# Kernel tuning notes

Hardware: AMD Instinct MI355X
Metric: run time of the kernel (lower is better)

## Reference

```python
import jax, jax.numpy as jnp
import numpy as np

NEG_SLOPE = 0.2


def setup_inputs() -> dict:
    key = jax.random.key(0)
    ks = jax.random.split(key, 12)
    N, D = 50000, 256
    H, C = 4, 128          # heads, per-head channels; H*C = gnn_hidden_dim = 512
    E = 800000
    edge_index = jax.random.randint(ks[0], (2, E), 0, N, dtype=jnp.int64)
    edge_weight = jax.random.uniform(ks[1], (E,), dtype=jnp.float32)
    s = 1.0 / np.sqrt(D)
    return {
        'edge_index': edge_index,
        'edge_weight': edge_weight,
        'emb':     jax.random.normal(ks[2], (N, D), jnp.float32),
        'W':       jax.random.normal(ks[3], (D, H * C), jnp.float32) * s,
        'att_src': jax.random.normal(ks[4], (H, C), jnp.float32) * s,
        'att_dst': jax.random.normal(ks[5], (H, C), jnp.float32) * s,
        'att_edge': jax.random.normal(ks[6], (H, C), jnp.float32) * s,
        'W_edge':  jax.random.normal(ks[7], (1, H * C), jnp.float32),
        'bias':    jnp.zeros((H * C,), jnp.float32),
        'W_out':   jax.random.normal(ks[8], (H * C, D), jnp.float32) * s,
        'b_out':   jnp.zeros((D,), jnp.float32),
    }


def reference(edge_index, edge_weight, emb, W, att_src, att_dst, att_edge,
              W_edge, bias, W_out, b_out):
    N, D = emb.shape
    H, C = att_src.shape
    src, dst = edge_index[0], edge_index[1]
    E = src.shape[0]

    # GATConv: shared linear projection for src and dst (in_channels is int)
    x = (emb @ W).reshape(N, H, C)                     # [N,H,C]

    # add self loops; edge_attr for loops = per-dst mean of incoming edge_attr
    ones = jnp.ones((E,), emb.dtype)
    cnt = jax.ops.segment_sum(ones, dst, num_segments=N)
    ea_mean = jax.ops.segment_sum(edge_weight, dst, num_segments=N) / jnp.maximum(cnt, 1.0)
    loop = jnp.arange(N, dtype=src.dtype)
    src_f = jnp.concatenate([src, loop])
    dst_f = jnp.concatenate([dst, loop])
    ea = jnp.concatenate([edge_weight, ea_mean])[:, None]   # [E+N, 1]

    e_feat = (ea @ W_edge).reshape(-1, H, C)            # [E+N,H,C]

    a_src = jnp.einsum('nhc,hc->nh', x, att_src)        # [N,H]
    a_dst = jnp.einsum('nhc,hc->nh', x, att_dst)
    a_e = jnp.einsum('ehc,hc->eh', e_feat, att_edge)    # [E+N,H]

    alpha = jax.nn.leaky_relu(a_src[src_f] + a_dst[dst_f] + a_e, NEG_SLOPE)
    # segment softmax over destination neighborhoods
    m = jax.ops.segment_max(alpha, dst_f, num_segments=N)
    alpha = jnp.exp(alpha - m[dst_f])
    denom = jax.ops.segment_sum(alpha, dst_f, num_segments=N)
    alpha = alpha / (denom[dst_f] + 1e-16)              # [E+N,H]

    msg = x[src_f] * alpha[..., None]                   # [E+N,H,C]
    out = jax.ops.segment_sum(msg, dst_f, num_segments=N).reshape(N, H * C) + bias

    return out @ W_out + b_out                          # [N,D]
```

## Files before the change

### kernel.cpp

```cpp
#include <hip/hip_runtime.h>
#include <cstdint>
#include <cstddef>

#define NEG_SLOPE 0.2f
#define HC 512
#define NH 4
#define CAP 64

typedef __attribute__((ext_vector_type(8))) short bf16x8;
typedef __attribute__((ext_vector_type(4))) float f32x4;

__device__ inline float lrelu(float z) { return z > 0.f ? z : NEG_SLOPE * z; }

__device__ inline unsigned short f2bf(float f) {
    unsigned u = __float_as_uint(f);
    u += 0x7FFFu + ((u >> 16) & 1u);
    return (unsigned short)(u >> 16);
}
__device__ inline float bflo(unsigned v) { return __uint_as_float(v << 16); }
__device__ inline float bfhi(unsigned v) { return __uint_as_float(v & 0xffff0000u); }

#define GLOAD16(gp, lp) \
    __builtin_amdgcn_global_load_lds( \
        (const __attribute__((address_space(1))) unsigned int*)(const void*)(gp), \
        (__attribute__((address_space(3))) unsigned int*)(void*)(lp), 16, 0, 0)

__global__ __launch_bounds__(256) void wprep_kernel(
        const float* __restrict__ W, const float* __restrict__ W_out,
        const float* __restrict__ att_s, const float* __restrict__ att_d,
        const float* __restrict__ W_edge, const float* __restrict__ att_edge,
        const float* __restrict__ bias, const float* __restrict__ b_out,
        const int* __restrict__ ei, const float* __restrict__ ew, int E,
        unsigned short* __restrict__ Wb, unsigned short* __restrict__ WoT,
        float* __restrict__ watt, float* __restrict__ bc4, float* __restrict__ sh,
        int* __restrict__ cnt, float* __restrict__ wsum, int2* __restrict__ csr2) {
    int b = blockIdx.x, t = threadIdx.x;
    if (b < 128) {
        int i = b * 256 + t;
        float4 v = reinterpret_cast<const float4*>(W)[i];
        ushort4 o;
        o.x = f2bf(v.x); o.y = f2bf(v.y); o.z = f2bf(v.z); o.w = f2bf(v.w);
        reinterpret_cast<ushort4*>(Wb)[i] = o;
    } else if (b < 640) {
        int idx = (b - 128) * 256 + t;
        int r = idx >> 8, c = idx & 255;
        WoT[(size_t)c * 512 + r] = f2bf(W_out[idx]);
    } else if (b < 648) {
        int i = b - 640;
        int h = i & 3;
        const float* att = (i < 4) ? att_s : att_d;
        float s = 0.f;
        for (int c = 0; c < 128; ++c)
            s += W[(size_t)t * HC + h * 128 + c] * att[h * 128 + c];
        watt[i * 256 + t] = s;
    } else if (b < 652) {
        int part = b - 648;
        int j0 = part * 128;
        float s = (part == 0) ? b_out[t] : 0.f;
        for (int j = j0; j < j0 + 128; ++j)
            s += bias[j] * W_out[(size_t)j * 256 + t];
        bc4[part * 256 + t] = s;
    } else if (b == 652) {
        if (t < NH) {
            float s = 0.f;
            for (int c = 0; c < 128; ++c)
                s += W_edge[t * 128 + c] * att_edge[t * 128 + c];
            sh[t] = s;
        }
    } else {
        int lane = t & 63;
        unsigned long long nzm = __ballot(ei[2 * lane + 1] != 0);
        int is64 = (nzm == 0ull) ? 1 : 0;
        int e = (b - 653) * 256 + t;
        if (e < E) {
            size_t de = (size_t)E + e;
            int d = is64 ? ei[2 * de] : ei[de];
            int s = is64 ? ei[2 * (size_t)e] : ei[e];
            float w = ew[e];
            int pos = atomicAdd(&cnt[d], 1);
            if (pos < CAP)
                csr2[(size_t)d * CAP + pos] = make_int2(s, __float_as_int(w));
            atomicAdd(&wsum[d], w);
        }
    }
}

__global__ __launch_bounds__(256) void mt_kernel(
        const unsigned short* __restrict__ WoT, const unsigned short* __restrict__ Wb,
        unsigned short* __restrict__ MT) {
    __shared__ __align__(16) unsigned short As[128 * 64];
    __shared__ __align__(16) unsigned short Bs[128 * 64];
    int b = blockIdx.x, t = threadIdx.x;
    int lane = t & 63, w = t >> 6;
    int bn = (b & 1) * 128, bm = ((b >> 1) & 1) * 128, z = b >> 2;
    const unsigned short* A  = WoT + (size_t)z * 128;
    const unsigned short* BT = Wb  + (size_t)z * 128;
    int wr = w >> 1, wc = w & 1;

    f32x4 acc[4][4];
    #pragma unroll
    for (int i = 0; i < 4; ++i)
        #pragma unroll
        for (int j = 0; j < 4; ++j)
            acc[i][j] = (f32x4){0.f, 0.f, 0.f, 0.f};

    int lr = lane & 15, kb = lane >> 4;
    int q = lane & 7;

    for (int k0 = 0; k0 < 128; k0 += 64) {
        #pragma unroll
        for (int p = 0; p < 4; ++p) {
            int row = p * 32 + w * 8 + (lane >> 3);
            int ce  = ((q ^ (row & 7)) << 3) + k0;
            int ob  = p * 4096 + w * 1024;
            GLOAD16(A  + (size_t)(bm + row) * 512 + ce, (char*)As + ob);
            GLOAD16(BT + (size_t)(bn + row) * 512 + ce, (char*)Bs + ob);
        }
        __syncthreads();
        #pragma unroll
        for (int kk = 0; kk < 2; ++kk) {
            bf16x8 a[4], bfr[4];
            #pragma unroll
            for (int i = 0; i < 4; ++i) {
                int row = wr * 64 + i * 16 + lr;
                a[i] = *reinterpret_cast<const bf16x8*>(
                    &As[row * 64 + (((kk * 4 + kb) ^ (row & 7)) << 3)]);
            }
            #pragma unroll
            for (int j = 0; j < 4; ++j) {
                int row = wc * 64 + j * 16 + lr;
                bfr[j] = *reinterpret_cast<const bf16x8*>(
                    &Bs[row * 64 + (((kk * 4 + kb) ^ (row & 7)) << 3)]);
            }
            #pragma unroll
            for (int i = 0; i < 4; ++i)
                #pragma unroll
                for (int j = 0; j < 4; ++j)
                    acc[i][j] = __builtin_amdgcn_mfma_f32_16x16x32_bf16(a[i], bfr[j], acc[i][j], 0, 0, 0);
        }
        __syncthreads();
    }
    int rg = lane >> 4;
    #pragma unroll
    for (int i = 0; i < 4; ++i)
        #pragma unroll
        for (int r = 0; r < 4; ++r) {
            int row = bm + wr * 64 + i * 16 + rg * 4 + r;
            #pragma unroll
            for (int j = 0; j < 4; ++j) {
                int col = bn + wc * 64 + j * 16 + lr;
                MT[(size_t)row * 1024 + z * 256 + col] = f2bf(acc[i][j][r]);
            }
        }
}

__global__ __launch_bounds__(256) void embcast_kernel(
        const float4* __restrict__ embf4, const float* __restrict__ watt,
        uint2* __restrict__ embq, float* __restrict__ a_src,
        float* __restrict__ a_dst, int N) {
    int t = threadIdx.x;
    int wid = t >> 6, lane = t & 63;
    #pragma unroll
    for (int j = 0; j < 4; ++j) {
        int n = blockIdx.x * 16 + wid * 4 + j;
        if (n >= N) break;
        float4 v = embf4[(size_t)n * 64 + lane];
        uint2 o;
        o.x = (unsigned)f2bf(v.x) | ((unsigned)f2bf(v.y) << 16);
        o.y = (unsigned)f2bf(v.z) | ((unsigned)f2bf(v.w) << 16);
        embq[(size_t)n * 64 + lane] = o;
        float r[8];
        #pragma unroll
        for (int i = 0; i < 8; ++i) {
            float4 wv = reinterpret_cast<const float4*>(watt)[i * 64 + lane];
            r[i] = v.x * wv.x + v.y * wv.y + v.z * wv.z + v.w * wv.w;
        }
        #pragma unroll
        for (int off = 32; off > 0; off >>= 1) {
            #pragma unroll
            for (int i = 0; i < 8; ++i) r[i] += __shfl_xor(r[i], off);
        }
        if (lane == 0) {
            size_t bofs = (size_t)n * 4;
            a_src[bofs + 0] = r[0]; a_src[bofs + 1] = r[1];
            a_src[bofs + 2] = r[2]; a_src[bofs + 3] = r[3];
            a_dst[bofs + 0] = r[4]; a_dst[bofs + 1] = r[5];
            a_dst[bofs + 2] = r[6]; a_dst[bofs + 3] = r[7];
        }
    }
}

#define EFMA(W_, V_) { \
    float e0_ = bflo(V_.x), e1_ = bfhi(V_.x), e2_ = bflo(V_.y), e3_ = bfhi(V_.y); \
    a00 += W_.x * e0_; a01 += W_.x * e1_; a02 += W_.x * e2_; a03 += W_.x * e3_; \
    a10 += W_.y * e0_; a11 += W_.y * e1_; a12 += W_.y * e2_; a13 += W_.y * e3_; \
    a20 += W_.z * e0_; a21 += W_.z * e1_; a22 += W_.z * e2_; a23 += W_.z * e3_; \
    a30 += W_.w * e0_; a31 += W_.w * e1_; a32 += W_.w * e2_; a33 += W_.w * e3_; \
    den0 += W_.x; den1 += W_.y; den2 += W_.z; den3 += W_.w; }

__global__ __launch_bounds__(256) void agg_kernel(
        const uint2* __restrict__ embq, const float* __restrict__ a_src,
        const float* __restrict__ a_dst, const int* __restrict__ cnt,
        const float* __restrict__ wsum, const float* __restrict__ sh,
        const int2* __restrict__ csr2, uint2* __restrict__ aggn, int N) {
    int wid = threadIdx.x >> 6, lane = threadIdx.x & 63;
    int n = blockIdx.x * 4 + wid;
    if (n >= N) return;
    int deg = cnt[n];
    float eam = wsum[n] / fmaxf((float)deg, 1.f);
    int m = deg < CAP ? deg : CAP;

    __shared__ int s_src[4][64];
    __shared__ __align__(16) float s_alpha[4][64][4];

    float ad0 = a_dst[(size_t)n * 4 + 0], ad1 = a_dst[(size_t)n * 4 + 1];
    float ad2 = a_dst[(size_t)n * 4 + 2], ad3 = a_dst[(size_t)n * 4 + 3];
    float sh0 = sh[0], sh1 = sh[1], sh2 = sh[2], sh3 = sh[3];
    float es0 = __expf(lrelu(a_src[(size_t)n * 4 + 0] + ad0 + eam * sh0));
    float es1 = __expf(lrelu(a_src[(size_t)n * 4 + 1] + ad1 + eam * sh1));
    float es2 = __expf(lrelu(a_src[(size_t)n * 4 + 2] + ad2 + eam * sh2));
    float es3 = __expf(lrelu(a_src[(size_t)n * 4 + 3] + ad3 + eam * sh3));

    uint2 xv = embq[(size_t)n * 64 + lane];
    float d0 = bflo(xv.x), d1 = bfhi(xv.x), d2 = bflo(xv.y), d3 = bfhi(xv.y);

    float a00 = es0 * d0, a01 = es0 * d1, a02 = es0 * d2, a03 = es0 * d3;
    float a10 = es1 * d0, a11 = es1 * d1, a12 = es1 * d2, a13 = es1 * d3;
    float a20 = es2 * d0, a21 = es2 * d1, a22 = es2 * d2, a23 = es2 * d3;
    float a30 = es3 * d0, a31 = es3 * d1, a32 = es3 * d2, a33 = es3 * d3;
    float den0 = es0, den1 = es1, den2 = es2, den3 = es3;

    if (lane < m) {
        int2 p = csr2[(size_t)n * CAP + lane];
        int s = p.x;
        float wgt = __int_as_float(p.y);
        s_src[wid][lane] = s;
        float4 as4 = *reinterpret_cast<const float4*>(&a_src[(size_t)s * 4]);
        s_alpha[wid][lane][0] = __expf(lrelu(as4.x + ad0 + wgt * sh0));
        s_alpha[wid][lane][1] = __expf(lrelu(as4.y + ad1 + wgt * sh1));
        s_alpha[wid][lane][2] = __expf(lrelu(as4.z + ad2 + wgt * sh2));
        s_alpha[wid][lane][3] = __expf(lrelu(as4.w + ad3 + wgt * sh3));
    }
    int e2 = 0;
    for (; e2 + 2 <= m; e2 += 2) {
        int s0 = s_src[wid][e2], s1 = s_src[wid][e2 + 1];
        float4 w0 = *reinterpret_cast<const float4*>(s_alpha[wid][e2]);
        float4 w1 = *reinterpret_cast<const float4*>(s_alpha[wid][e2 + 1]);
        uint2 v0 = embq[(size_t)s0 * 64 + lane];
        uint2 v1 = embq[(size_t)s1 * 64 + lane];
        EFMA(w0, v0); EFMA(w1, v1);
    }
    if (e2 < m) {
        int s0 = s_src[wid][e2];
        float4 w0 = *reinterpret_cast<const float4*>(s_alpha[wid][e2]);
        uint2 v0 = embq[(size_t)s0 * 64 + lane];
        EFMA(w0, v0);
    }

    float i0 = 1.f / (den0 + 1e-16f), i1 = 1.f / (den1 + 1e-16f);
    float i2 = 1.f / (den2 + 1e-16f), i3 = 1.f / (den3 + 1e-16f);
    size_t base = (size_t)n * 256 + lane;
    uint2 o;
    o.x = (unsigned)f2bf(a00 * i0) | ((unsigned)f2bf(a01 * i0) << 16);
    o.y = (unsigned)f2bf(a02 * i0) | ((unsigned)f2bf(a03 * i0) << 16);
    aggn[base] = o;
    o.x = (unsigned)f2bf(a10 * i1) | ((unsigned)f2bf(a11 * i1) << 16);
    o.y = (unsigned)f2bf(a12 * i1) | ((unsigned)f2bf(a13 * i1) << 16);
    aggn[base + 64] = o;
    o.x = (unsigned)f2bf(a20 * i2) | ((unsigned)f2bf(a21 * i2) << 16);
    o.y = (unsigned)f2bf(a22 * i2) | ((unsigned)f2bf(a23 * i2) << 16);
    aggn[base + 128] = o;
    o.x = (unsigned)f2bf(a30 * i3) | ((unsigned)f2bf(a31 * i3) << 16);
    o.y = (unsigned)f2bf(a32 * i3) | ((unsigned)f2bf(a33 * i3) << 16);
    aggn[base + 192] = o;
}

__global__ __launch_bounds__(512) void gemm_out_kernel(
        const unsigned short* __restrict__ A,
        const unsigned short* __restrict__ BT,
        const float* __restrict__ bc4, float* __restrict__ C, int M) {
    __shared__ __align__(16) unsigned short As[128 * 64];
    __shared__ __align__(16) unsigned short Bs[256 * 64];
    int tid = threadIdx.x;
    int lane = tid & 63, w = tid >> 6;
    int bm = blockIdx.x * 128;
    int wr = w >> 2, wc = w & 3;

    f32x4 acc[4][4];
    #pragma unroll
    for (int i = 0; i < 4; ++i)
        #pragma unroll
        for (int j = 0; j < 4; ++j)
            acc[i][j] = (f32x4){0.f, 0.f, 0.f, 0.f};

    int lr = lane & 15, kb = lane >> 4;
    int q = lane & 7;

    for (int k0 = 0; k0 < 1024; k0 += 64) {
        #pragma unroll
        for (int p = 0; p < 2; ++p) {
            int row = p * 64 + w * 8 + (lane >> 3);
            int ce  = ((q ^ (row & 7)) << 3) + k0;
            int ob  = p * 8192 + w * 1024;
            int gr = bm + row; if (gr >= M) gr = M - 1;
            GLOAD16(A + (size_t)gr * 1024 + ce, (char*)As + ob);
        }
        #pragma unroll
        for (int p = 0; p < 4; ++p) {
            int row = p * 64 + w * 8 + (lane >> 3);
            int ce  = ((q ^ (row & 7)) << 3) + k0;
            int ob  = p * 8192 + w * 1024;
            GLOAD16(BT + (size_t)row * 1024 + ce, (char*)Bs + ob);
        }
        __syncthreads();

        #pragma unroll
        for (int kk = 0; kk < 2; ++kk) {
            bf16x8 a[4], b[4];
            #pragma unroll
            for (int i = 0; i < 4; ++i) {
                int row = wr * 64 + i * 16 + lr;
                a[i] = *reinterpret_cast<const bf16x8*>(
                    &As[row * 64 + (((kk * 4 + kb) ^ (row & 7)) << 3)]);
            }
            #pragma unroll
            for (int j = 0; j < 4; ++j) {
                int row = wc * 64 + j * 16 + lr;
                b[j] = *reinterpret_cast<const bf16x8*>(
                    &Bs[row * 64 + (((kk * 4 + kb) ^ (row & 7)) << 3)]);
            }
            #pragma unroll
            for (int i = 0; i < 4; ++i)
                #pragma unroll
                for (int j = 0; j < 4; ++j)
                    acc[i][j] = __builtin_amdgcn_mfma_f32_16x16x32_bf16(a[i], b[j], acc[i][j], 0, 0, 0);
        }
        __syncthreads();
    }

    int rg = lane >> 4;
    #pragma unroll
    for (int i = 0; i < 4; ++i) {
        #pragma unroll
        for (int r = 0; r < 4; ++r) {
            int row = bm + wr * 64 + i * 16 + rg * 4 + r;
            if (row >= M) continue;
            #pragma unroll
            for (int j = 0; j < 4; ++j) {
                int col = wc * 64 + j * 16 + lr;
                float bval = bc4[col] + bc4[256 + col] + bc4[512 + col] + bc4[768 + col];
                C[(size_t)row * 256 + col] = acc[i][j][r] + bval;
            }
        }
    }
}

extern "C" void kernel_launch(void* const* d_in, const int* in_sizes, int n_in,
                              void* d_out, int out_size, void* d_ws, size_t ws_size,
                              hipStream_t stream) {
    const int*   edge_index  = (const int*)d_in[0];
    const float* edge_weight = (const float*)d_in[1];
    const float* emb         = (const float*)d_in[2];
    const float* W           = (const float*)d_in[3];
    const float* att_src     = (const float*)d_in[4];
    const float* att_dst     = (const float*)d_in[5];
    const float* att_edge    = (const float*)d_in[6];
    const float* W_edge      = (const float*)d_in[7];
    const float* bias        = (const float*)d_in[8];
    const float* W_out       = (const float*)d_in[9];
    const float* b_out       = (const float*)d_in[10];
    float* out = (float*)d_out;

    const int E = in_sizes[1];
    const int D = 256;
    const int N = in_sizes[2] / D;
    const int mb = (N + 127) / 128;
    const int nEmb = (N + 15) / 16;
    const int nEdge = (E + 255) / 256;

    char* ws = (char*)d_ws;
    size_t off = 0;
    auto alloc = [&](size_t bytes) {
        size_t o = off;
        off += (bytes + 255) & ~(size_t)255;
        return o;
    };
    unsigned short* embb  = (unsigned short*)(ws + alloc((size_t)N * D * 2));
    unsigned short* aggn  = (unsigned short*)(ws + alloc((size_t)N * 1024 * 2));
    unsigned short* Wb    = (unsigned short*)(ws + alloc((size_t)D * HC * 2));
    unsigned short* WoT   = (unsigned short*)(ws + alloc((size_t)HC * D * 2));
    unsigned short* MT    = (unsigned short*)(ws + alloc((size_t)256 * 1024 * 2));
    float* watt    = (float*)(ws + alloc(2048 * 4));
    float* bc4     = (float*)(ws + alloc(1024 * 4));
    float* a_src   = (float*)(ws + alloc((size_t)N * 4 * 4));
    float* a_dst   = (float*)(ws + alloc((size_t)N * 4 * 4));
    float* sh      = (float*)(ws + alloc(64));
    size_t zbytes  = (size_t)N * 8;
    size_t zoff    = alloc(zbytes);
    int*   cnt     = (int*)(ws + zoff);
    float* wsum    = (float*)(ws + zoff + (size_t)N * 4);
    int2*  csr2    = (int2*)(ws + alloc((size_t)N * CAP * 8));
    (void)ws_size; (void)n_in; (void)out_size;

    hipMemsetAsync(ws + zoff, 0, zbytes, stream);

    wprep_kernel<<<653 + nEdge, 256, 0, stream>>>(
        W, W_out, att_src, att_dst, W_edge, att_edge, bias, b_out,
        edge_index, edge_weight, E, Wb, WoT, watt, bc4, sh, cnt, wsum, csr2);

    mt_kernel<<<16, 256, 0, stream>>>(WoT, Wb, MT);

    embcast_kernel<<<nEmb, 256, 0, stream>>>(
        (const float4*)emb, watt, (uint2*)embb, a_src, a_dst, N);

    agg_kernel<<<(N + 3) / 4, 256, 0, stream>>>(
        (const uint2*)embb, a_src, a_dst, cnt, wsum, sh, csr2,
        (uint2*)aggn, N);

    gemm_out_kernel<<<mb, 512, 0, stream>>>(aggn, MT, bc4, out, N);
}
```

Measured before the change: 262.7 us.

## Drop float atomic weight-sum; recompute mean in aggregation via wave reduction

The edge scatter no longer does a float atomicAdd into a per-destination weight sum. Each aggregation wave instead reduces the weights of its CSR bucket with a shuffle reduction to get the self-loop mean. The scatter kernel also handles four edges per thread, issuing all loads before the atomics to raise memory-level parallelism, and the memset shrinks. Risk: when a node has more than CAP incoming edges, the mean now covers only the stored edges while still dividing by the full degree, so results differ from the reference in that case.

```diff
diff --git a/kernel.cpp b/kernel.cpp
--- a/kernel.cpp
+++ b/kernel.cpp
@@ -33,7 +33,7 @@
         const int* __restrict__ ei, const float* __restrict__ ew, int E,
         unsigned short* __restrict__ Wb, unsigned short* __restrict__ WoT,
         float* __restrict__ watt, float* __restrict__ bc4, float* __restrict__ sh,
-        int* __restrict__ cnt, float* __restrict__ wsum, int2* __restrict__ csr2) {
+        int* __restrict__ cnt, int2* __restrict__ csr2) {
     int b = blockIdx.x, t = threadIdx.x;
     if (b < 128) {
         int i = b * 256 + t;
@@ -71,17 +71,31 @@
         int lane = t & 63;
         unsigned long long nzm = __ballot(ei[2 * lane + 1] != 0);
         int is64 = (nzm == 0ull) ? 1 : 0;
-        int e = (b - 653) * 256 + t;
-        if (e < E) {
-            size_t de = (size_t)E + e;
-            int d = is64 ? ei[2 * de] : ei[de];
-            int s = is64 ? ei[2 * (size_t)e] : ei[e];
-            float w = ew[e];
-            int pos = atomicAdd(&cnt[d], 1);
-            if (pos < CAP)
-                csr2[(size_t)d * CAP + pos] = make_int2(s, __float_as_int(w));
-            atomicAdd(&wsum[d], w);
-        }
+        int base = (b - 653) * 1024;
+
+        int dv[4], sv[4];
+        float wv[4];
+        bool ok[4];
+        #pragma unroll
+        for (int r = 0; r < 4; ++r) {
+            int e = base + r * 256 + t;
+            ok[r] = (e < E);
+            if (ok[r]) {
+                size_t de = (size_t)E + e;
+                dv[r] = is64 ? ei[2 * de] : ei[de];
+                sv[r] = is64 ? ei[2 * (size_t)e] : ei[e];
+                wv[r] = ew[e];
+            }
+        }
+        int pos[4];
+        #pragma unroll
+        for (int r = 0; r < 4; ++r)
+            if (ok[r]) pos[r] = atomicAdd(&cnt[dv[r]], 1);
+        #pragma unroll
+        for (int r = 0; r < 4; ++r)
+            if (ok[r] && pos[r] < CAP)
+                csr2[(size_t)dv[r] * CAP + pos[r]] =
+                    make_int2(sv[r], __float_as_int(wv[r]));
     }
 }
 
@@ -201,17 +215,27 @@
 __global__ __launch_bounds__(256) void agg_kernel(
         const uint2* __restrict__ embq, const float* __restrict__ a_src,
         const float* __restrict__ a_dst, const int* __restrict__ cnt,
-        const float* __restrict__ wsum, const float* __restrict__ sh,
-        const int2* __restrict__ csr2, uint2* __restrict__ aggn, int N) {
+        const float* __restrict__ sh, const int2* __restrict__ csr2,
+        uint2* __restrict__ aggn, int N) {
     int wid = threadIdx.x >> 6, lane = threadIdx.x & 63;
     int n = blockIdx.x * 4 + wid;
     if (n >= N) return;
     int deg = cnt[n];
-    float eam = wsum[n] / fmaxf((float)deg, 1.f);
     int m = deg < CAP ? deg : CAP;
 
     __shared__ int s_src[4][64];
     __shared__ __align__(16) float s_alpha[4][64][4];
+
+    int2 p;
+    float wgt = 0.f;
+    if (lane < m) {
+        p = csr2[(size_t)n * CAP + lane];
+        wgt = __int_as_float(p.y);
+    }
+    float wsl = wgt;
+    #pragma unroll
+    for (int o = 32; o > 0; o >>= 1) wsl += __shfl_xor(wsl, o);
+    float eam = wsl / fmaxf((float)deg, 1.f);
 
     float ad0 = a_dst[(size_t)n * 4 + 0], ad1 = a_dst[(size_t)n * 4 + 1];
     float ad2 = a_dst[(size_t)n * 4 + 2], ad3 = a_dst[(size_t)n * 4 + 3];
@@ -231,9 +255,7 @@
     float den0 = es0, den1 = es1, den2 = es2, den3 = es3;
 
     if (lane < m) {
-        int2 p = csr2[(size_t)n * CAP + lane];
         int s = p.x;
-        float wgt = __int_as_float(p.y);
         s_src[wid][lane] = s;
         float4 as4 = *reinterpret_cast<const float4*>(&a_src[(size_t)s * 4]);
         s_alpha[wid][lane][0] = __expf(lrelu(as4.x + ad0 + wgt * sh0));
@@ -376,7 +398,7 @@
     const int N = in_sizes[2] / D;
     const int mb = (N + 127) / 128;
     const int nEmb = (N + 15) / 16;
-    const int nEdge = (E + 255) / 256;
+    const int nEdge4 = (E + 1023) / 1024;
 
     char* ws = (char*)d_ws;
     size_t off = 0;
@@ -395,18 +417,17 @@
     float* a_src   = (float*)(ws + alloc((size_t)N * 4 * 4));
     float* a_dst   = (float*)(ws + alloc((size_t)N * 4 * 4));
     float* sh      = (float*)(ws + alloc(64));
-    size_t zbytes  = (size_t)N * 8;
+    size_t zbytes  = (size_t)N * 4;
     size_t zoff    = alloc(zbytes);
     int*   cnt     = (int*)(ws + zoff);
-    float* wsum    = (float*)(ws + zoff + (size_t)N * 4);
     int2*  csr2    = (int2*)(ws + alloc((size_t)N * CAP * 8));
     (void)ws_size; (void)n_in; (void)out_size;
 
     hipMemsetAsync(ws + zoff, 0, zbytes, stream);
 
-    wprep_kernel<<<653 + nEdge, 256, 0, stream>>>(
+    wprep_kernel<<<653 + nEdge4, 256, 0, stream>>>(
         W, W_out, att_src, att_dst, W_edge, att_edge, bias, b_out,
-        edge_index, edge_weight, E, Wb, WoT, watt, bc4, sh, cnt, wsum, csr2);
+        edge_index, edge_weight, E, Wb, WoT, watt, bc4, sh, cnt, csr2);
 
     mt_kernel<<<16, 256, 0, stream>>>(WoT, Wb, MT);
 
@@ -414,8 +435,7 @@
         (const float4*)emb, watt, (uint2*)embb, a_src, a_dst, N);
 
     agg_kernel<<<(N + 3) / 4, 256, 0, stream>>>(
-        (const uint2*)embb, a_src, a_dst, cnt, wsum, sh, csr2,
-        (uint2*)aggn, N);
+        (const uint2*)embb, a_src, a_dst, cnt, sh, csr2, (uint2*)aggn, N);
 
     gemm_out_kernel<<<mb, 512, 0, stream>>>(aggn, MT, bc4, out, N);
 }
```

Result: faster. 226.5 us (-13.8%).
